# Kernel optimization log

Hardware: AMD Instinct MI355X
Metric: run time of the kernel (lower is better)

Reference implementation:

```python
import jax, jax.numpy as jnp
import numpy as np
from jax.scipy.linalg import expm

B, T = 32, 4096
FREQ_DIM = 128
HID = 64
OUT_DIM = 2
N_COMP = 4
DT = 0.1
EPS = 1e-5


def setup_inputs() -> dict:
    key = jax.random.key(0)
    ks = jax.random.split(key, 16)
    f32 = jnp.float32

    def lin(k, out_d, in_d):
        bound = 1.0 / np.sqrt(in_d)
        kw, kb = jax.random.split(k)
        W = jax.random.uniform(kw, (out_d, in_d), f32, -bound, bound)
        b = jax.random.uniform(kb, (out_d,), f32, -bound, bound)
        return W, b

    x = jax.random.normal(ks[0], (B, T, 1), f32)
    # EnhancedWavePhysics params
    freq_spectrum = jnp.linspace(1.0, 20.0, FREQ_DIM, dtype=f32)
    pm_w1, pm_b1 = lin(ks[1], 128, 1)
    pm_w2, pm_b2 = lin(ks[2], FREQ_DIM * 2, 128)
    wc_w, wc_b = lin(ks[3], HID, FREQ_DIM)
    amp_ctrl = jnp.ones((1,), f32) * 0.1
    # quantum encoder
    qe_w1, qe_b1 = lin(ks[4], HID * 2, HID)
    qe_w2, qe_b2 = lin(ks[5], HID * 4, HID * 2)
    # layernorm
    ln_g = jnp.ones((HID * 4,), f32)
    ln_b = jnp.zeros((HID * 4,), f32)
    # skew-symmetric hamiltonians [4, 64, 64]
    A = jax.random.normal(ks[6], (N_COMP, HID, HID), f32) * 0.05
    hams = (A - jnp.swapaxes(A, -1, -2)) / 2.0
    # interference net
    int_w1, int_b1 = lin(ks[7], 32, 4)
    int_w2, int_b2 = lin(ks[8], OUT_DIM, 32)
    int_strength = jnp.ones((1,), f32)
    return dict(x=x, freq_spectrum=freq_spectrum, pm_w1=pm_w1, pm_b1=pm_b1,
                pm_w2=pm_w2, pm_b2=pm_b2, wc_w=wc_w, wc_b=wc_b,
                amp_ctrl=amp_ctrl, qe_w1=qe_w1, qe_b1=qe_b1, qe_w2=qe_w2,
                qe_b2=qe_b2, ln_g=ln_g, ln_b=ln_b, hams=hams,
                int_w1=int_w1, int_b1=int_b1, int_w2=int_w2, int_b2=int_b2,
                int_strength=int_strength)


def reference(x, freq_spectrum, pm_w1, pm_b1, pm_w2, pm_b2, wc_w, wc_b,
              amp_ctrl, qe_w1, qe_b1, qe_w2, qe_b2, ln_g, ln_b, hams,
              int_w1, int_b1, int_w2, int_b2, int_strength):
    Bx, Tx, _ = x.shape
    # --- EnhancedWavePhysics ---
    mod = jnp.tanh(x @ pm_w1.T + pm_b1) @ pm_w2.T + pm_b2            # [B,T,2F]
    amplitude, phase = jnp.split(mod, 2, axis=-1)                     # [B,T,F]
    amplitude = jnp.tanh(amplitude) * amp_ctrl
    time = jnp.linspace(0.0, 2.0 * np.pi, Tx)[None, :, None]          # [1,T,1]
    freqs = freq_spectrum[None, None, :]                              # [1,1,F]
    wave_components = amplitude * jnp.sin(freqs * time + phase)       # [B,T,F]
    wave_field = jnp.tanh(wave_components @ wc_w.T + wc_b)            # [B,T,H]
    # --- quantum encoder + layernorm ---
    q = jnp.tanh(wave_field @ qe_w1.T + qe_b1) @ qe_w2.T + qe_b2      # [B,T,4H]
    mu = q.mean(-1, keepdims=True)
    var = q.var(-1, keepdims=True)
    q = (q - mu) / jnp.sqrt(var + EPS) * ln_g + ln_b
    psi = q.reshape(Bx, Tx, N_COMP, HID)                              # [B,T,C,D]
    # --- Hamiltonian evolution: torch does matrix_exp(-1j*(1j*H)*dt)=expm(H*dt)
    #     (H skew-symmetric real => U real orthogonal), then psi @ U.T, take real.
    U = jax.vmap(expm)(hams * DT)                                     # [C,D,D]
    evolved = jnp.einsum('btcd,ced->btce', psi, U)                    # [B,T,C,D]
    # --- EnhancedInterference ---
    spec = jnp.abs(jnp.fft.fft(evolved, axis=1))                      # [B,T,C,D]
    freq_w = jax.nn.softmax(spec.mean(-1), axis=1)                    # [B,T,C]
    weighted = jnp.sum(spec * freq_w[..., None], axis=1)              # [B,C,D]
    spatial_avg = weighted.mean(-1)                                   # [B,C]
    out = jnp.tanh(spatial_avg @ int_w1.T + int_b1) @ int_w2.T + int_b2
    return out * int_strength                                         # [B,out_dim]
```

## Files before the change

kernel.cpp:

```cpp
#include <hip/hip_runtime.h>
#include <hip/hip_bf16.h>

#define TT 4096
#define BB 32

typedef unsigned short ushort_t;
typedef __attribute__((ext_vector_type(8))) short short8v;
typedef __attribute__((ext_vector_type(4))) float float4v;

__device__ inline ushort_t bf16rn(float v) {
    unsigned u = __float_as_uint(v);
    unsigned r = (u + 0x7FFFu + ((u >> 16) & 1u)) >> 16;
    return (ushort_t)r;
}
__device__ inline float bf16tof(ushort_t h) {
    return __uint_as_float(((unsigned)h) << 16);
}
__device__ inline int SW(int i) { return i + (i >> 5); }

__device__ inline float fast_tanh(float x) {
    float e = __builtin_amdgcn_exp2f(x * 2.8853900817779268f);
    return 1.0f - 2.0f * __builtin_amdgcn_rcpf(e + 1.0f);
}
__device__ inline float fast_sin(float x) {
    return __builtin_amdgcn_sinf(x * 0.15915494309189535f);
}

__global__ __launch_bounds__(256) void k1_expm(const float* __restrict__ hams,
                                               ushort_t* __restrict__ Uhi,
                                               ushort_t* __restrict__ Ulo)
{
    int c = blockIdx.x, tid = threadIdx.x;
    __shared__ float M[4096], P[4096], Acc[4096];
    const float* H = hams + c * 4096;
    for (int k = tid; k < 4096; k += 256) {
        float m = H[k] * 0.1f;
        M[k] = m; P[k] = m;
        Acc[k] = m + (((k >> 6) == (k & 63)) ? 1.0f : 0.0f);
    }
    __syncthreads();
    int j = tid & 63;
    float mcol[64];
    #pragma unroll
    for (int k = 0; k < 64; k++) mcol[k] = M[k * 64 + j];
    for (int term = 2; term <= 8; term++) {
        float inv = 1.0f / (float)term;
        float np_[16];
        #pragma unroll
        for (int r = 0; r < 16; r++) {
            int i = (tid >> 6) + 4 * r;
            float a = 0.f;
            #pragma unroll
            for (int k = 0; k < 64; k++) a = fmaf(P[i * 64 + k], mcol[k], a);
            np_[r] = a * inv;
        }
        __syncthreads();
        #pragma unroll
        for (int r = 0; r < 16; r++) {
            int i = (tid >> 6) + 4 * r;
            P[i * 64 + j] = np_[r];
            Acc[i * 64 + j] += np_[r];
        }
        __syncthreads();
    }
    for (int k = tid; k < 4096; k += 256) {
        float v = Acc[k];
        ushort_t h = bf16rn(v);
        Uhi[c * 4096 + k] = h;
        Ulo[c * 4096 + k] = bf16rn(v - bf16tof(h));
    }
}

__global__ void split_all(const float* __restrict__ pw2, const float* __restrict__ wcw,
                          const float* __restrict__ qw1, const float* __restrict__ qw2,
                          ushort_t* __restrict__ wb)
{
    int i = blockIdx.x * 256 + threadIdx.x;
    const float* src; ushort_t *hi, *lo; int off;
    if (i < 32768)      { src = pw2; hi = wb;          lo = wb + 32768;  off = i; }
    else if (i < 40960) { src = wcw; hi = wb + 65536;  lo = wb + 73728;  off = i - 32768; }
    else if (i < 49152) { src = qw1; hi = wb + 81920;  lo = wb + 90112;  off = i - 40960; }
    else                { src = qw2; hi = wb + 98304;  lo = wb + 131072; off = i - 49152; }
    float v = src[off];
    ushort_t h = bf16rn(v);
    hi[off] = h;
    lo[off] = bf16rn(v - bf16tof(h));
}

__global__ __launch_bounds__(256, 2) void gemm_s1(
    const ushort_t* __restrict__ Whi, const ushort_t* __restrict__ Wlo,
    const float* __restrict__ bias,
    const float* __restrict__ x, const float* __restrict__ pw1,
    const float* __restrict__ pb1,
    const float* __restrict__ freq, const float* __restrict__ ampc,
    ushort_t* __restrict__ O)
{
    __shared__ ushort_t OT[2][2048];
    int tid = threadIdx.x;
    int w = tid >> 6, l = tid & 63, l15 = l & 15, kg = l >> 4;
    int kofb = kg * 8;

    short8v bh[4][4], bl[4][4];
    #pragma unroll
    for (int i = 0; i < 4; i++) {
        int n = (w + 4 * i) * 16 + l15;
        #pragma unroll
        for (int kc = 0; kc < 4; kc++) {
            int kof = kc * 32 + kofb;
            bh[i][kc] = *(const short8v*)(Whi + (size_t)n * 128 + kof);
            bl[i][kc] = *(const short8v*)(Wlo + (size_t)n * 128 + kof);
        }
    }
    float am = ampc[0];
    float fr[2], ba[2], bp[2];
    #pragma unroll
    for (int i = 0; i < 2; i++) {
        int f = (w + 4 * i) * 16 + l15;
        fr[i] = freq[f]; ba[i] = bias[f]; bp[i] = bias[128 + f];
    }

    int mbase = blockIdx.x * 64;
    for (int mi = 0; mi < 4; mi++) {
        int m0 = mbase + mi * 16;
        float xv = x[m0 + l15];
        short8v ah[4], al[4];
        #pragma unroll
        for (int kc = 0; kc < 4; kc++) {
            int k0 = kc * 32 + kofb;
            float4 w0 = *(const float4*)(pw1 + k0);
            float4 w1v = *(const float4*)(pw1 + k0 + 4);
            float4 b0 = *(const float4*)(pb1 + k0);
            float4 b1v = *(const float4*)(pb1 + k0 + 4);
            #pragma unroll
            for (int j = 0; j < 8; j++) {
                float wj = (j < 4) ? (&w0.x)[j] : (&w1v.x)[j - 4];
                float bj = (j < 4) ? (&b0.x)[j] : (&b1v.x)[j - 4];
                float v = fast_tanh(fmaf(xv, wj, bj));
                ushort_t h = bf16rn(v);
                ah[kc][j] = (short)h;
                al[kc][j] = (short)bf16rn(v - bf16tof(h));
            }
        }
        float4v acc[4];
        #pragma unroll
        for (int i = 0; i < 4; i++) acc[i] = (float4v){0.f, 0.f, 0.f, 0.f};
        #pragma unroll
        for (int kc = 0; kc < 4; kc++) {
            #pragma unroll
            for (int i = 0; i < 4; i++) {
                acc[i] = __builtin_amdgcn_mfma_f32_16x16x32_bf16(ah[kc], bh[i][kc], acc[i], 0, 0, 0);
                acc[i] = __builtin_amdgcn_mfma_f32_16x16x32_bf16(ah[kc], bl[i][kc], acc[i], 0, 0, 0);
                acc[i] = __builtin_amdgcn_mfma_f32_16x16x32_bf16(al[kc], bh[i][kc], acc[i], 0, 0, 0);
            }
        }
        int buf = mi & 1;
        #pragma unroll
        for (int i = 0; i < 2; i++) {
            int f = (w + 4 * i) * 16 + l15;
            #pragma unroll
            for (int r = 0; r < 4; r++) {
                int m = m0 + kg * 4 + r;
                float timev = 6.283185307179586f * (float)(m & 4095) / 4095.0f;
                float a = fast_tanh(acc[i][r] + ba[i]) * am;
                float ph = acc[i + 2][r] + bp[i];
                float v = a * fast_sin(fmaf(fr[i], timev, ph));
                OT[buf][(kg * 4 + r) * 128 + f] = bf16rn(v);
            }
        }
        __syncthreads();
        *(uint4*)(O + (size_t)m0 * 128 + tid * 8) = *(const uint4*)(&OT[buf][tid * 8]);
    }
}

__global__ __launch_bounds__(256, 2) void s23_v2(
    const ushort_t* __restrict__ A,
    const ushort_t* __restrict__ W2hi, const ushort_t* __restrict__ W2lo,
    const float* __restrict__ b2,
    const ushort_t* __restrict__ W3hi, const ushort_t* __restrict__ W3lo,
    const float* __restrict__ b3,
    ushort_t* __restrict__ OHi, ushort_t* __restrict__ OLo)
{
    __shared__ unsigned WF[2][16][65];
    __shared__ ushort_t OThi[2][2048], OTlo[2][2048];
    int tid = threadIdx.x;
    int w = tid >> 6, l = tid & 63, l15 = l & 15, kg = l >> 4;
    int kofb = kg * 8;

    short8v w2h[4], w2l[4];
    #pragma unroll
    for (int kc = 0; kc < 4; kc++) {
        int n = w * 16 + l15;
        int kof = kc * 32 + kofb;
        w2h[kc] = *(const short8v*)(W2hi + (size_t)n * 128 + kof);
        w2l[kc] = *(const short8v*)(W2lo + (size_t)n * 128 + kof);
    }
    short8v w3h[2][2], w3l[2][2];
    #pragma unroll
    for (int i = 0; i < 2; i++) {
        int n = (w + 4 * i) * 16 + l15;
        #pragma unroll
        for (int kc = 0; kc < 2; kc++) {
            int kof = kc * 32 + kofb;
            w3h[i][kc] = *(const short8v*)(W3hi + (size_t)n * 64 + kof);
            w3l[i][kc] = *(const short8v*)(W3lo + (size_t)n * 64 + kof);
        }
    }
    float b2v = b2[w * 16 + l15];
    float b3v[2];
    #pragma unroll
    for (int i = 0; i < 2; i++) b3v[i] = b3[(w + 4 * i) * 16 + l15];

    int mbase = blockIdx.x * 64;
    for (int mi = 0; mi < 4; mi++) {
        int m0 = mbase + mi * 16;
        short8v ah[4];
        #pragma unroll
        for (int kc = 0; kc < 4; kc++) {
            int kof = kc * 32 + kofb;
            ah[kc] = *(const short8v*)(A + (size_t)(m0 + l15) * 128 + kof);
        }
        float4v acc1 = (float4v){0.f, 0.f, 0.f, 0.f};
        #pragma unroll
        for (int kc = 0; kc < 4; kc++) {
            acc1 = __builtin_amdgcn_mfma_f32_16x16x32_bf16(ah[kc], w2h[kc], acc1, 0, 0, 0);
            acc1 = __builtin_amdgcn_mfma_f32_16x16x32_bf16(ah[kc], w2l[kc], acc1, 0, 0, 0);
        }
        int buf = mi & 1;
        #pragma unroll
        for (int r = 0; r < 4; r++) {
            float v = fast_tanh(acc1[r] + b2v);
            ushort_t h = bf16rn(v);
            ushort_t lo2 = bf16rn(v - bf16tof(h));
            WF[buf][kg * 4 + r][w * 16 + l15] = (unsigned)h | ((unsigned)lo2 << 16);
        }
        __syncthreads();
        float4v acc2[2];
        acc2[0] = (float4v){0.f, 0.f, 0.f, 0.f};
        acc2[1] = (float4v){0.f, 0.f, 0.f, 0.f};
        #pragma unroll
        for (int kc = 0; kc < 2; kc++) {
            short8v a2h, a2l;
            #pragma unroll
            for (int j = 0; j < 8; j++) {
                unsigned u = WF[buf][l15][kc * 32 + kofb + j];
                a2h[j] = (short)(u & 0xFFFFu);
                a2l[j] = (short)(u >> 16);
            }
            #pragma unroll
            for (int i = 0; i < 2; i++) {
                acc2[i] = __builtin_amdgcn_mfma_f32_16x16x32_bf16(a2h, w3h[i][kc], acc2[i], 0, 0, 0);
                acc2[i] = __builtin_amdgcn_mfma_f32_16x16x32_bf16(a2h, w3l[i][kc], acc2[i], 0, 0, 0);
                acc2[i] = __builtin_amdgcn_mfma_f32_16x16x32_bf16(a2l, w3h[i][kc], acc2[i], 0, 0, 0);
            }
        }
        #pragma unroll
        for (int i = 0; i < 2; i++) {
            int n = (w + 4 * i) * 16 + l15;
            #pragma unroll
            for (int r = 0; r < 4; r++) {
                float v = fast_tanh(acc2[i][r] + b3v[i]);
                ushort_t h = bf16rn(v);
                OThi[buf][(kg * 4 + r) * 128 + n] = h;
                OTlo[buf][(kg * 4 + r) * 128 + n] = bf16rn(v - bf16tof(h));
            }
        }
        __syncthreads();
        *(uint4*)(OHi + (size_t)m0 * 128 + tid * 8) = *(const uint4*)(&OThi[buf][tid * 8]);
        *(uint4*)(OLo + (size_t)m0 * 128 + tid * 8) = *(const uint4*)(&OTlo[buf][tid * 8]);
    }
}

__global__ __launch_bounds__(256, 2) void gemm_s4e(
    const ushort_t* __restrict__ Ahi, const ushort_t* __restrict__ Alo,
    const ushort_t* __restrict__ Whi, const ushort_t* __restrict__ Wlo,
    const float* __restrict__ bias,
    const float* __restrict__ lng, const float* __restrict__ lnb,
    const ushort_t* __restrict__ Uhi, const ushort_t* __restrict__ Ulo,
    unsigned* __restrict__ psiu)
{
    __shared__ float partS[2][4][16], partSS[2][4][16];
    __shared__ unsigned PT[256 * 33];
    int tid = threadIdx.x;
    int w = tid >> 6, l = tid & 63, l15 = l & 15, kg = l >> 4;
    int kofb = kg * 8;

    short8v bh[4][4], bl[4][4];
    #pragma unroll
    for (int i = 0; i < 4; i++) {
        int n = (w + 4 * i) * 16 + l15;
        #pragma unroll
        for (int kc = 0; kc < 4; kc++) {
            int kof = kc * 32 + kofb;
            bh[i][kc] = *(const short8v*)(Whi + (size_t)n * 128 + kof);
            bl[i][kc] = *(const short8v*)(Wlo + (size_t)n * 128 + kof);
        }
    }
    float bv[4], g4[4], be4[4];
    #pragma unroll
    for (int i = 0; i < 4; i++) {
        int n = (w + 4 * i) * 16 + l15;
        bv[i] = bias[n]; g4[i] = lng[n]; be4[i] = lnb[n];
    }

    int mbase = blockIdx.x * 32;
    int b = mbase >> 12, tbase = mbase & 4095;
    for (int mi = 0; mi < 2; mi++) {
        int m0 = mbase + mi * 16;
        short8v ah[4], al[4];
        #pragma unroll
        for (int kc = 0; kc < 4; kc++) {
            int kof = kc * 32 + kofb;
            ah[kc] = *(const short8v*)(Ahi + (size_t)(m0 + l15) * 128 + kof);
            al[kc] = *(const short8v*)(Alo + (size_t)(m0 + l15) * 128 + kof);
        }
        float4v acc[4];
        #pragma unroll
        for (int i = 0; i < 4; i++) acc[i] = (float4v){0.f, 0.f, 0.f, 0.f};
        #pragma unroll
        for (int kc = 0; kc < 4; kc++) {
            #pragma unroll
            for (int i = 0; i < 4; i++) {
                acc[i] = __builtin_amdgcn_mfma_f32_16x16x32_bf16(ah[kc], bh[i][kc], acc[i], 0, 0, 0);
                acc[i] = __builtin_amdgcn_mfma_f32_16x16x32_bf16(ah[kc], bl[i][kc], acc[i], 0, 0, 0);
                acc[i] = __builtin_amdgcn_mfma_f32_16x16x32_bf16(al[kc], bh[i][kc], acc[i], 0, 0, 0);
            }
        }
        float s[4] = {0, 0, 0, 0}, ss[4] = {0, 0, 0, 0};
        #pragma unroll
        for (int i = 0; i < 4; i++) {
            #pragma unroll
            for (int r = 0; r < 4; r++) {
                float v = acc[i][r] + bv[i];
                s[r] += v; ss[r] += v * v;
            }
        }
        #pragma unroll
        for (int r = 0; r < 4; r++) {
            #pragma unroll
            for (int off = 1; off < 16; off <<= 1) {
                s[r] += __shfl_xor(s[r], off);
                ss[r] += __shfl_xor(ss[r], off);
            }
        }
        int pb_ = mi & 1;
        if (l15 == 0) {
            #pragma unroll
            for (int r = 0; r < 4; r++) {
                partS[pb_][w][kg * 4 + r] = s[r];
                partSS[pb_][w][kg * 4 + r] = ss[r];
            }
        }
        __syncthreads();
        float mu[4], rstd[4];
        #pragma unroll
        for (int r = 0; r < 4; r++) {
            float ts = 0.f, tss = 0.f;
            #pragma unroll
            for (int wv = 0; wv < 4; wv++) {
                ts += partS[pb_][wv][kg * 4 + r];
                tss += partSS[pb_][wv][kg * 4 + r];
            }
            mu[r] = ts * (1.0f / 256.0f);
            float var = tss * (1.0f / 256.0f) - mu[r] * mu[r];
            rstd[r] = rsqrtf(var + 1e-5f);
        }
        #pragma unroll
        for (int i = 0; i < 4; i++) {
            int n = (w + 4 * i) * 16 + l15;
            #pragma unroll
            for (int r = 0; r < 4; r++) {
                float v = (acc[i][r] + bv[i] - mu[r]) * rstd[r] * g4[i] + be4[i];
                ushort_t h = bf16rn(v);
                ushort_t lo2 = bf16rn(v - bf16tof(h));
                PT[n * 33 + mi * 16 + kg * 4 + r] = (unsigned)h | ((unsigned)lo2 << 16);
            }
        }
    }
    __syncthreads();

    int c = w;
    size_t gb = ((size_t)(b * 256 + c * 64)) * 4096 + tbase;
    for (int et = 0; et < 4; et++) {
        short8v ua_h[2], ua_l[2];
        #pragma unroll
        for (int kc = 0; kc < 2; kc++) {
            size_t uo = (size_t)c * 4096 + (et * 16 + l15) * 64 + kc * 32 + kofb;
            ua_h[kc] = *(const short8v*)(Uhi + uo);
            ua_l[kc] = *(const short8v*)(Ulo + uo);
        }
        #pragma unroll
        for (int tt = 0; tt < 2; tt++) {
            float4v acc = (float4v){0.f, 0.f, 0.f, 0.f};
            #pragma unroll
            for (int kc = 0; kc < 2; kc++) {
                short8v b_h, b_l;
                #pragma unroll
                for (int j = 0; j < 8; j++) {
                    unsigned u = PT[(c * 64 + kc * 32 + kofb + j) * 33 + tt * 16 + l15];
                    b_h[j] = (short)(u & 0xFFFFu);
                    b_l[j] = (short)(u >> 16);
                }
                acc = __builtin_amdgcn_mfma_f32_16x16x32_bf16(ua_h[kc], b_h, acc, 0, 0, 0);
                acc = __builtin_amdgcn_mfma_f32_16x16x32_bf16(ua_h[kc], b_l, acc, 0, 0, 0);
                acc = __builtin_amdgcn_mfma_f32_16x16x32_bf16(ua_l[kc], b_h, acc, 0, 0, 0);
            }
            #pragma unroll
            for (int r = 0; r < 4; r++) {
                int e = et * 16 + kg * 4 + r;
                float v = acc[r];
                ushort_t h = bf16rn(v);
                ushort_t lo2 = bf16rn(v - bf16tof(h));
                psiu[gb + (size_t)e * 4096 + tt * 16 + l15] =
                    (unsigned)h | ((unsigned)lo2 << 16);
            }
        }
    }
}

__global__ __launch_bounds__(256, 2) void k3b_fft(const unsigned* __restrict__ ev,
                                                  float* __restrict__ msum8)
{
    __shared__ float re[4224], im[4224];
    int b = blockIdx.x, c = blockIdx.y, g = blockIdx.z;
    int tid = threadIdx.x;

    float macc[8];
    #pragma unroll
    for (int r = 0; r < 8; r++) macc[r] = 0.f;
    float macc8 = 0.f;

    size_t base = (((size_t)b * 4 + c) * 64 + (size_t)g * 8) * TT;
    for (int p = 0; p < 4; p++) {
        __syncthreads();
        for (int r = 0; r < 4; r++) {
            int t0 = (r * 256 + tid) * 4;
            uint4 va = *(const uint4*)(ev + base + (size_t)(2 * p) * TT + t0);
            uint4 vb = *(const uint4*)(ev + base + (size_t)(2 * p + 1) * TT + t0);
            #pragma unroll
            for (int j = 0; j < 4; j++) {
                int rv = __brev((unsigned)(t0 + j)) >> 20;
                unsigned ua = (&va.x)[j], ub = (&vb.x)[j];
                re[SW(rv)] = bf16tof((ushort_t)(ua & 0xFFFFu)) + bf16tof((ushort_t)(ua >> 16));
                im[SW(rv)] = bf16tof((ushort_t)(ub & 0xFFFFu)) + bf16tof((ushort_t)(ub >> 16));
            }
        }
        __syncthreads();

        #pragma unroll
        for (int trip = 0; trip < 3; trip++) {
            const int sh = trip * 4;
            int pos = tid & ((1 << sh) - 1);
            int grp = tid >> sh;
            int i0 = (grp << (sh + 4)) + pos;

            float yr[16], yi[16];
            #pragma unroll
            for (int j = 0; j < 16; j++) {
                int a = SW(i0 + (j << sh));
                yr[j] = re[a]; yi[j] = im[a];
            }
            float ang = -(float)pos / (float)(16 << sh);
            float t1r = __builtin_amdgcn_cosf(ang);
            float t1i = __builtin_amdgcn_sinf(ang);
            float t2r = t1r * t1r - t1i * t1i, t2i = 2.f * t1r * t1i;
            float t4r = t2r * t2r - t2i * t2i, t4i = 2.f * t2r * t2i;
            float t8r = t4r * t4r - t4i * t4i, t8i = 2.f * t4r * t4i;

            #pragma unroll
            for (int m = 0; m < 8; m++) {
                int j0 = 2 * m, j1 = j0 + 1;
                float tr = t8r * yr[j1] - t8i * yi[j1];
                float ti = t8r * yi[j1] + t8i * yr[j1];
                yr[j1] = yr[j0] - tr; yi[j1] = yi[j0] - ti;
                yr[j0] += tr;         yi[j0] += ti;
            }
            #pragma unroll
            for (int bs = 0; bs < 16; bs += 4) {
                {
                    int j0 = bs, j1 = bs + 2;
                    float tr = t4r * yr[j1] - t4i * yi[j1];
                    float ti = t4r * yi[j1] + t4i * yr[j1];
                    yr[j1] = yr[j0] - tr; yi[j1] = yi[j0] - ti;
                    yr[j0] += tr;         yi[j0] += ti;
                }
                {
                    int j0 = bs + 1, j1 = bs + 3;
                    float tr = t4i * yr[j1] + t4r * yi[j1];
                    float ti = t4i * yi[j1] - t4r * yr[j1];
                    yr[j1] = yr[j0] - tr; yi[j1] = yi[j0] - ti;
                    yr[j0] += tr;         yi[j0] += ti;
                }
            }
            {
                float wr = t2r, wi = t2i;
                #pragma unroll
                for (int j = 0; j < 4; j++) {
                    #pragma unroll
                    for (int bs = 0; bs < 16; bs += 8) {
                        int j0 = bs + j, j1 = j0 + 4;
                        float tr = wr * yr[j1] - wi * yi[j1];
                        float ti = wr * yi[j1] + wi * yr[j1];
                        yr[j1] = yr[j0] - tr; yi[j1] = yi[j0] - ti;
                        yr[j0] += tr;         yi[j0] += ti;
                    }
                    float nwr = (wr + wi) * 0.70710678f;
                    float nwi = (wi - wr) * 0.70710678f;
                    wr = nwr; wi = nwi;
                }
            }
            {
                float wr = t1r, wi = t1i;
                #pragma unroll
                for (int j = 0; j < 8; j++) {
                    int j0 = j, j1 = j + 8;
                    float tr = wr * yr[j1] - wi * yi[j1];
                    float ti = wr * yi[j1] + wi * yr[j1];
                    yr[j1] = yr[j0] - tr; yi[j1] = yi[j0] - ti;
                    yr[j0] += tr;         yi[j0] += ti;
                    float nwr = wr * 0.92387953f + wi * 0.38268343f;
                    float nwi = wi * 0.92387953f - wr * 0.38268343f;
                    wr = nwr; wi = nwi;
                }
            }
            #pragma unroll
            for (int j = 0; j < 16; j++) {
                int a = SW(i0 + (j << sh));
                re[a] = yr[j]; im[a] = yi[j];
            }
            __syncthreads();
        }

        for (int r = 0; r < 8; r++) {
            int k = tid + r * 256;
            int mk = (4096 - k) & 4095;
            float rk = re[SW(k)], ik = im[SW(k)];
            float rm = re[SW(mk)], imm = im[SW(mk)];
            float dA1 = rk + rm, dA2 = ik - imm;
            float dB1 = ik + imm, dB2 = rk - rm;
            float magA = 0.5f * sqrtf(dA1 * dA1 + dA2 * dA2);
            float magB = 0.5f * sqrtf(dB1 * dB1 + dB2 * dB2);
            macc[r] += magA + magB;
        }
        if (tid == 0) {
            float rk = re[SW(2048)], ik = im[SW(2048)];
            macc8 += fabsf(rk) + fabsf(ik);
        }
    }
    float* ms = msum8 + (((size_t)b * 4 + c) * 8 + g) * 4096;
    for (int r = 0; r < 8; r++) {
        int k = tid + r * 256;
        ms[k] = macc[r];
        if (k > 0) ms[4096 - k] = macc[r];
    }
    if (tid == 0) ms[2048] = macc8;
}

__global__ __launch_bounds__(256) void k4_softdot(const float* __restrict__ msum8,
                                                  float* __restrict__ sa)
{
    __shared__ float m[4096];
    __shared__ float red[256];
    int bc = blockIdx.x, tid = threadIdx.x;
    const float* ms = msum8 + (size_t)bc * 8 * 4096;
    float lmax = -1e30f;
    for (int k = tid; k < 4096; k += 256) {
        float v = 0.f;
        #pragma unroll
        for (int g = 0; g < 8; g++) v += ms[g * 4096 + k];
        v *= (1.0f / 64.0f);
        m[k] = v;
        lmax = fmaxf(lmax, v);
    }
    red[tid] = lmax; __syncthreads();
    for (int s2 = 128; s2 > 0; s2 >>= 1) {
        if (tid < s2) red[tid] = fmaxf(red[tid], red[tid + s2]);
        __syncthreads();
    }
    float mx = red[0]; __syncthreads();
    float lsum = 0.f, ldot = 0.f;
    for (int k = tid; k < 4096; k += 256) {
        float e = expf(m[k] - mx);
        lsum += e; ldot += e * m[k];
    }
    red[tid] = lsum; __syncthreads();
    for (int s2 = 128; s2 > 0; s2 >>= 1) {
        if (tid < s2) red[tid] += red[tid + s2];
        __syncthreads();
    }
    float tsum = red[0]; __syncthreads();
    red[tid] = ldot; __syncthreads();
    for (int s2 = 128; s2 > 0; s2 >>= 1) {
        if (tid < s2) red[tid] += red[tid + s2];
        __syncthreads();
    }
    if (tid == 0) sa[bc] = red[0] / tsum;
}

__global__ void k5_head(const float* __restrict__ sa,
                        const float* __restrict__ w1, const float* __restrict__ b1,
                        const float* __restrict__ w2, const float* __restrict__ b2,
                        const float* __restrict__ strength,
                        float* __restrict__ out)
{
    int b = threadIdx.x;
    if (b >= 32) return;
    float s0 = sa[b * 4 + 0], s1 = sa[b * 4 + 1];
    float s2 = sa[b * 4 + 2], s3 = sa[b * 4 + 3];
    float h[32];
    #pragma unroll
    for (int j = 0; j < 32; j++)
        h[j] = tanhf(b1[j] + w1[j * 4 + 0] * s0 + w1[j * 4 + 1] * s1 +
                     w1[j * 4 + 2] * s2 + w1[j * 4 + 3] * s3);
    float st = strength[0];
    #pragma unroll
    for (int o = 0; o < 2; o++) {
        float a = b2[o];
        #pragma unroll
        for (int j = 0; j < 32; j++) a = fmaf(w2[o * 32 + j], h[j], a);
        out[b * 2 + o] = a * st;
    }
}

extern "C" void kernel_launch(void* const* d_in, const int* in_sizes, int n_in,
                              void* d_out, int out_size, void* d_ws, size_t ws_size,
                              hipStream_t stream)
{
    const float* x    = (const float*)d_in[0];
    const float* freq = (const float*)d_in[1];
    const float* pw1  = (const float*)d_in[2];
    const float* pb1  = (const float*)d_in[3];
    const float* pw2  = (const float*)d_in[4];
    const float* pb2  = (const float*)d_in[5];
    const float* wcw  = (const float*)d_in[6];
    const float* wcb  = (const float*)d_in[7];
    const float* ampc = (const float*)d_in[8];
    const float* qw1  = (const float*)d_in[9];
    const float* qb1  = (const float*)d_in[10];
    const float* qw2  = (const float*)d_in[11];
    const float* qb2  = (const float*)d_in[12];
    const float* lng  = (const float*)d_in[13];
    const float* lnb  = (const float*)d_in[14];
    const float* hams = (const float*)d_in[15];
    const float* iw1  = (const float*)d_in[16];
    const float* ib1  = (const float*)d_in[17];
    const float* iw2  = (const float*)d_in[18];
    const float* ib2  = (const float*)d_in[19];
    const float* istr = (const float*)d_in[20];

    char* wsb = (char*)d_ws;
    ushort_t* AHi = (ushort_t*)(wsb + 0);
    ushort_t* ALo = (ushort_t*)(wsb + 33554432);
    ushort_t* Bwcf = (ushort_t*)(wsb + 67108864);
    unsigned* psi = (unsigned*)(wsb + 67108864);
    float*    msum8 = (float*)(wsb + 0);
    ushort_t* Uhi  = (ushort_t*)(wsb + 201326592);
    ushort_t* Ulo  = (ushort_t*)(wsb + 201359360);
    float*    sa   = (float*)(wsb + 201392128);
    ushort_t* wb   = (ushort_t*)(wsb + 203489792);
    ushort_t *pw2hi = wb,          *pw2lo = wb + 32768;
    ushort_t *wcwhi = wb + 65536,  *wcwlo = wb + 73728;
    ushort_t *qw1hi = wb + 81920,  *qw1lo = wb + 90112;
    ushort_t *qw2hi = wb + 98304,  *qw2lo = wb + 131072;
    float* out = (float*)d_out;

    k1_expm<<<4, 256, 0, stream>>>(hams, Uhi, Ulo);
    split_all<<<320, 256, 0, stream>>>(pw2, wcw, qw1, qw2, wb);

    gemm_s1<<<2048, 256, 0, stream>>>(pw2hi, pw2lo, pb2, x, pw1, pb1,
                                      freq, ampc, Bwcf);
    s23_v2<<<2048, 256, 0, stream>>>(Bwcf, wcwhi, wcwlo, wcb,
        qw1hi, qw1lo, qb1, AHi, ALo);
    gemm_s4e<<<4096, 256, 0, stream>>>(AHi, ALo, qw2hi, qw2lo, qb2,
        lng, lnb, Uhi, Ulo, psi);

    k3b_fft<<<dim3(32, 4, 8), 256, 0, stream>>>(psi, msum8);
    k4_softdot<<<128, 256, 0, stream>>>(msum8, sa);
    k5_head<<<1, 64, 0, stream>>>(sa, iw1, ib1, iw2, ib2, istr, out);
}
```

Baseline: 391.0 us.

## Stage evolved outputs in shared memory and store them as coalesced time-blocked tiles

```diff
diff --git a/kernel.cpp b/kernel.cpp
--- a/kernel.cpp
+++ b/kernel.cpp
@@ -379,7 +379,8 @@
     __syncthreads();
 
     int c = w;
-    size_t gb = ((size_t)(b * 256 + c * 64)) * 4096 + tbase;
+    unsigned outv[32];
+    #pragma unroll
     for (int et = 0; et < 4; et++) {
         short8v ua_h[2], ua_l[2];
         #pragma unroll
@@ -406,14 +407,38 @@
             }
             #pragma unroll
             for (int r = 0; r < 4; r++) {
-                int e = et * 16 + kg * 4 + r;
                 float v = acc[r];
                 ushort_t h = bf16rn(v);
                 ushort_t lo2 = bf16rn(v - bf16tof(h));
-                psiu[gb + (size_t)e * 4096 + tt * 16 + l15] =
-                    (unsigned)h | ((unsigned)lo2 << 16);
-            }
-        }
+                outv[et * 8 + tt * 4 + r] = (unsigned)h | ((unsigned)lo2 << 16);
+            }
+        }
+    }
+    #pragma unroll
+    for (int et = 0; et < 4; et++) {
+        #pragma unroll
+        for (int tt = 0; tt < 2; tt++) {
+            #pragma unroll
+            for (int r = 0; r < 4; r++) {
+                int e = et * 16 + kg * 4 + r;
+                PT[(c * 64 + e) * 33 + tt * 16 + l15] = outv[et * 8 + tt * 4 + r];
+            }
+        }
+    }
+    __syncthreads();
+
+    int tb = tbase >> 5;
+    unsigned* dst = psiu + ((size_t)(b * 128 + tb)) * 8192;
+    #pragma unroll
+    for (int j = 0; j < 8; j++) {
+        int idx = j * 1024 + tid * 4;
+        int ce = idx >> 5, tl = idx & 31;
+        uint4 v;
+        v.x = PT[ce * 33 + tl];
+        v.y = PT[ce * 33 + tl + 1];
+        v.z = PT[ce * 33 + tl + 2];
+        v.w = PT[ce * 33 + tl + 3];
+        *(uint4*)(dst + idx) = v;
     }
 }
 
@@ -429,13 +454,16 @@
     for (int r = 0; r < 8; r++) macc[r] = 0.f;
     float macc8 = 0.f;
 
-    size_t base = (((size_t)b * 4 + c) * 64 + (size_t)g * 8) * TT;
+    size_t bbase = (size_t)b * 128 * 8192;
+    int ce0 = c * 64 + g * 8;
     for (int p = 0; p < 4; p++) {
         __syncthreads();
         for (int r = 0; r < 4; r++) {
             int t0 = (r * 256 + tid) * 4;
-            uint4 va = *(const uint4*)(ev + base + (size_t)(2 * p) * TT + t0);
-            uint4 vb = *(const uint4*)(ev + base + (size_t)(2 * p + 1) * TT + t0);
+            int tb = t0 >> 5, tl = t0 & 31;
+            size_t chunk = bbase + (size_t)tb * 8192 + tl;
+            uint4 va = *(const uint4*)(ev + chunk + (ce0 + 2 * p) * 32);
+            uint4 vb = *(const uint4*)(ev + chunk + (ce0 + 2 * p + 1) * 32);
             #pragma unroll
             for (int j = 0; j < 4; j++) {
                 int rv = __brev((unsigned)(t0 + j)) >> 20;
```

New measurement: 392.3 us. Within noise of the previous version (+0.3%).
